# Kernel optimization log

Hardware: AMD Instinct MI355X
Metric: run time of the kernel (lower is better)

The kernel has to match this reference:

```python
import jax, jax.numpy as jnp
import numpy as np

EMBED = 384
N_HEADS = 6
HEAD_SIZE = EMBED // N_HEADS
B, T = 4, 2048
EPS = 1e-5


def _layernorm(x, g, b):
    mu = jnp.mean(x, axis=-1, keepdims=True)
    var = jnp.mean(jnp.square(x - mu), axis=-1, keepdims=True)
    return (x - mu) * jax.lax.rsqrt(var + EPS) * g + b


def setup_inputs() -> dict:
    key = jax.random.key(0)
    ks = jax.random.split(key, 6)
    s = 0.02
    return {
        "x": jax.random.normal(ks[0], (B, T, EMBED), jnp.float32),
        "Wq": jax.random.normal(ks[1], (N_HEADS, HEAD_SIZE, EMBED), jnp.float32) * s,
        "Wo": jax.random.normal(ks[2], (EMBED, EMBED), jnp.float32) * s,
        "bo": jnp.zeros((EMBED,), jnp.float32),
        "W1": jax.random.normal(ks[3], (EMBED, EMBED), jnp.float32) * s,
        "b1": jnp.zeros((EMBED,), jnp.float32),
        "W2": jax.random.normal(ks[4], (EMBED, EMBED), jnp.float32) * s,
        "b2": jnp.zeros((EMBED,), jnp.float32),
        "g1": jnp.ones((EMBED,), jnp.float32),
        "be1": jnp.zeros((EMBED,), jnp.float32),
        "g2": jnp.ones((EMBED,), jnp.float32),
        "be2": jnp.zeros((EMBED,), jnp.float32),
    }


def reference(x, Wq, Wo, bo, W1, b1, W2, b2, g1, be1, g2, be2):
    # NOTE: original Head uses self.query for q, k AND v (a bug we reproduce):
    # q = k = v = x @ Wq^T per head.
    q = jnp.einsum("bte,hde->bhtd", x, Wq)  # [B,H,T,D]
    scale = HEAD_SIZE ** -0.5
    scores = jnp.einsum("bhtd,bhsd->bhts", q, q) * scale  # [B,H,T,T]
    # torch.tril zeros the upper triangle, then masked_fill(tmp==0, -inf)
    tril = jnp.tril(jnp.ones((T, T), bool))
    scores = jnp.where(tril, scores, 0.0)
    scores = jnp.where(scores == 0.0, -jnp.inf, scores)
    attn = jax.nn.softmax(scores, axis=-1)
    head_out = jnp.einsum("bhts,bhsd->bhtd", attn, q)  # [B,H,T,D]
    cat = head_out.transpose(0, 2, 1, 3).reshape(B, T, EMBED)  # concat heads
    sa = cat @ Wo.T + bo
    x = _layernorm(x + sa, g1, be1)
    ff = jax.nn.relu(x @ W1.T + b1) @ W2.T + b2
    return _layernorm(x + ff, g2, be2)
```

## Files before the change

kernel.cpp:

```cpp
#include <hip/hip_runtime.h>
#include <math.h>

#define BB 4
#define TT 2048
#define EE 384
#define HH 6
#define DD 64
#define MM (BB*TT)

typedef __attribute__((ext_vector_type(8))) short bf16x8;
typedef __attribute__((ext_vector_type(4))) float f32x4;

__device__ __forceinline__ unsigned short f2bf(float f) {
    unsigned int u = __float_as_uint(f);
    u = (u + 0x7FFFu + ((u >> 16) & 1u)) >> 16;
    return (unsigned short)u;
}
__device__ __forceinline__ float bf2f(unsigned short u) {
    return __uint_as_float(((unsigned int)u) << 16);
}
__device__ __forceinline__ unsigned int pk2(float a, float b) {
    return (unsigned int)f2bf(a) | ((unsigned int)f2bf(b) << 16);
}
__device__ __forceinline__ unsigned int cvtpk(float lo, float hi) {
    unsigned int r;
    asm("v_cvt_pk_bf16_f32 %0, %1, %2" : "=v"(r) : "v"(lo), "v"(hi));
    return r;
}

__global__ __launch_bounds__(256) void k_cvt(const float* __restrict__ wq,
                                             const float* __restrict__ wo,
                                             const float* __restrict__ w1,
                                             const float* __restrict__ w2,
                                             unsigned short* __restrict__ wqb,
                                             unsigned short* __restrict__ wob,
                                             unsigned short* __restrict__ w1b,
                                             unsigned short* __restrict__ w2b)
{
    int wi = blockIdx.x / 144, off = (blockIdx.x % 144) * 256;
    const float* s4[4] = {wq, wo, w1, w2};
    unsigned short* d4[4] = {wqb, wob, w1b, w2b};
    const float* src = s4[wi]; unsigned short* dst = d4[wi];
    int i = off + threadIdx.x;
    float4 v = ((const float4*)src)[i];
    uint2 o; o.x = pk2(v.x, v.y); o.y = pk2(v.z, v.w);
    ((uint2*)dst)[i] = o;
}

__global__ __launch_bounds__(256, 2) void k_qgemm(const float* __restrict__ x,
                                                  const unsigned short* __restrict__ W,
                                                  unsigned short* __restrict__ qbf,
                                                  unsigned short* __restrict__ qbfT)
{
    __shared__ unsigned short Xs[32][396];
    __shared__ unsigned short Ts[32][200];
    const int tid = threadIdx.x;
    const int w = tid >> 6, lane = tid & 63;
    const int fr = lane & 15, quad = lane >> 4;
    const int m0 = blockIdx.x * 32;
    const int n0 = blockIdx.y * 192 + w * 48;
    const unsigned short* Wp = W + (size_t)(n0 + fr) * EE + quad * 8;

    {
        const float* xp = x + (size_t)m0 * EE;
        #pragma unroll
        for (int it = 0; it < 12; it++) {
            int idx = it * 1024 + tid * 4;
            int row = idx / EE, col = idx % EE;
            float4 v = *(const float4*)(xp + idx);
            uint2 o; o.x = pk2(v.x, v.y); o.y = pk2(v.z, v.w);
            *(uint2*)&Xs[row][col] = o;
        }
    }

    f32x4 acc[2][3];
    bf16x8 bc[3], bn[3];
    #pragma unroll
    for (int mt = 0; mt < 2; mt++)
        #pragma unroll
        for (int nt = 0; nt < 3; nt++) acc[mt][nt] = (f32x4){0.f, 0.f, 0.f, 0.f};
    #pragma unroll
    for (int nt = 0; nt < 3; nt++) bc[nt] = *(const bf16x8*)(Wp + (size_t)nt * 16 * EE);
    __syncthreads();

    #pragma unroll
    for (int k0 = 0; k0 < 12; k0++) {
        if (k0 < 11) {
            #pragma unroll
            for (int nt = 0; nt < 3; nt++)
                bn[nt] = *(const bf16x8*)(Wp + (size_t)nt * 16 * EE + (k0 + 1) * 32);
        }
        bf16x8 a0 = *(const bf16x8*)&Xs[fr][k0 * 32 + quad * 8];
        bf16x8 a1 = *(const bf16x8*)&Xs[16 + fr][k0 * 32 + quad * 8];
        #pragma unroll
        for (int nt = 0; nt < 3; nt++) {
            acc[0][nt] = __builtin_amdgcn_mfma_f32_16x16x32_bf16(a0, bc[nt], acc[0][nt], 0, 0, 0);
            acc[1][nt] = __builtin_amdgcn_mfma_f32_16x16x32_bf16(a1, bc[nt], acc[1][nt], 0, 0, 0);
        }
        #pragma unroll
        for (int nt = 0; nt < 3; nt++) bc[nt] = bn[nt];
    }

    const int bglob = m0 >> 11, t0 = m0 & 2047;
    #pragma unroll
    for (int nt = 0; nt < 3; nt++) {
        int nl = w * 48 + nt * 16 + fr;
        int n = blockIdx.y * 192 + nl;
        int h = n >> 6, d = n & 63;
        #pragma unroll
        for (int mt = 0; mt < 2; mt++)
            #pragma unroll
            for (int r = 0; r < 4; r++) {
                int ml = mt * 16 + quad * 4 + r;
                unsigned short bf = f2bf(acc[mt][nt][r]);
                qbf[((size_t)(bglob * HH + h) * TT + t0 + ml) * DD + d] = bf;
                Ts[ml][nl] = bf;
            }
    }
    __syncthreads();
    if (tid < 192) {
        int nl = tid;
        int n = blockIdx.y * 192 + nl;
        int h = n >> 6, d = n & 63;
        unsigned short tmp[32];
        #pragma unroll
        for (int i = 0; i < 32; i++) tmp[i] = Ts[i][nl];
        unsigned short* dst = qbfT + ((size_t)(bglob * HH + h) * DD + d) * TT + t0;
        *(uint4*)(dst)      = *(const uint4*)&tmp[0];
        *(uint4*)(dst + 8)  = *(const uint4*)&tmp[8];
        *(uint4*)(dst + 16) = *(const uint4*)&tmp[16];
        *(uint4*)(dst + 24) = *(const uint4*)&tmp[24];
    }
}

__global__ __launch_bounds__(256, 4) void k_attn(const unsigned short* __restrict__ qbf,
                                                 const unsigned short* __restrict__ qbfT,
                                                 unsigned short* __restrict__ cat)
{
    __shared__ unsigned short Ks[2][64][72];
    __shared__ unsigned short Vs[2][64][72];
    __shared__ unsigned short Ps[32][72];
    __shared__ float lsc[32];
    float (*Oc)[68] = (float(*)[68])&Ks[0][0][0];

    const int id = blockIdx.x;
    const int xcd = id & 7, j = id >> 3;
    const int bh = xcd * 3 + (j % 3);
    const int p = j / 3;
    const int bb = bh / HH, hh = bh % HH;
    const int tid = threadIdx.x;
    const int w = tid >> 6, lane = tid & 63;
    const int qhalf = w & 1, keyhalf = w >> 1;
    const int fr = lane & 15, quad = lane >> 4;
    const int fc = quad * 8;
    const unsigned short* qb  = qbf  + (size_t)bh * TT * DD;
    const unsigned short* qtb = qbfT + (size_t)bh * DD * TT;
    const int lr = tid >> 2, lc = (tid & 3) * 16;
    const float EXSC = 0.18033688011112042f;

    #pragma unroll 1
    for (int ph = 0; ph < 2; ph++) {
        const int tile = ph ? (63 - p) : p;
        const int m0 = tile * 32;
        const int nkt = (tile >> 1) + 1;

        uint4 kr0, kr1, vr0, vr1;
        {
            const unsigned short* kp = qb + (size_t)lr * DD + lc;
            kr0 = *(const uint4*)(kp);
            kr1 = *(const uint4*)(kp + 8);
            const unsigned short* vp = qtb + (size_t)lr * TT + lc;
            vr0 = *(const uint4*)(vp);
            vr1 = *(const uint4*)(vp + 8);
        }
        const unsigned short* qp = qb + (size_t)(m0 + qhalf * 16 + fr) * DD + fc;
        const bf16x8 qA0 = *(const bf16x8*)(qp);
        const bf16x8 qA1 = *(const bf16x8*)(qp + 32);

        __syncthreads();
        *(uint4*)&Ks[0][lr][lc]     = kr0;
        *(uint4*)&Ks[0][lr][lc + 8] = kr1;
        *(uint4*)&Vs[0][lr][lc]     = vr0;
        *(uint4*)&Vs[0][lr][lc + 8] = vr1;
        __syncthreads();

        f32x4 accO[4];
        #pragma unroll
        for (int dt = 0; dt < 4; dt++) accO[dt] = (f32x4){0.f, 0.f, 0.f, 0.f};
        float ls[4] = {0.f, 0.f, 0.f, 0.f};
        const int rowbase = m0 + qhalf * 16 + quad * 4;
        const int prow = qhalf * 16 + quad * 4;

        for (int kt = 0; kt < nkt; kt++) {
            const int cur = kt & 1;
            const int s0 = kt * 64;
            if (kt < nkt - 1) {
                const unsigned short* kp = qb + (size_t)(s0 + 64 + lr) * DD + lc;
                kr0 = *(const uint4*)(kp);
                kr1 = *(const uint4*)(kp + 8);
                const unsigned short* vp = qtb + (size_t)lr * TT + s0 + 64 + lc;
                vr0 = *(const uint4*)(vp);
                vr1 = *(const uint4*)(vp + 8);
            }

            f32x4 S[2];
            #pragma unroll
            for (int nt = 0; nt < 2; nt++) {
                f32x4 acc = (f32x4){0.f, 0.f, 0.f, 0.f};
                bf16x8 b0 = *(const bf16x8*)&Ks[cur][keyhalf * 32 + nt * 16 + fr][fc];
                acc = __builtin_amdgcn_mfma_f32_16x16x32_bf16(qA0, b0, acc, 0, 0, 0);
                bf16x8 b1 = *(const bf16x8*)&Ks[cur][keyhalf * 32 + nt * 16 + fr][fc + 32];
                acc = __builtin_amdgcn_mfma_f32_16x16x32_bf16(qA1, b1, acc, 0, 0, 0);
                S[nt] = acc;
            }

            const bool edge = (kt == nkt - 1);
            #pragma unroll
            for (int nt = 0; nt < 2; nt++) {
                const int col = keyhalf * 32 + nt * 16 + fr;
                float pv[4];
                if (edge) {
                    const int jg = s0 + col;
                    #pragma unroll
                    for (int r = 0; r < 4; r++) {
                        float s = S[nt][r];
                        pv[r] = (jg <= rowbase + r && s != 0.0f)
                                ? __builtin_amdgcn_exp2f(s * EXSC) : 0.0f;
                        ls[r] += pv[r];
                    }
                } else {
                    #pragma unroll
                    for (int r = 0; r < 4; r++) {
                        float s = S[nt][r];
                        pv[r] = (s != 0.0f) ? __builtin_amdgcn_exp2f(s * EXSC) : 0.0f;
                        ls[r] += pv[r];
                    }
                }
                unsigned int pk0 = cvtpk(pv[0], pv[1]);
                unsigned int pk1 = cvtpk(pv[2], pv[3]);
                Ps[prow + 0][col] = (unsigned short)(pk0);
                Ps[prow + 1][col] = (unsigned short)(pk0 >> 16);
                Ps[prow + 2][col] = (unsigned short)(pk1);
                Ps[prow + 3][col] = (unsigned short)(pk1 >> 16);
            }

            bf16x8 pA = *(const bf16x8*)&Ps[qhalf * 16 + fr][keyhalf * 32 + fc];
            #pragma unroll
            for (int dt = 0; dt < 4; dt++) {
                bf16x8 v0 = *(const bf16x8*)&Vs[cur][dt * 16 + fr][keyhalf * 32 + fc];
                accO[dt] = __builtin_amdgcn_mfma_f32_16x16x32_bf16(pA, v0, accO[dt], 0, 0, 0);
            }

            if (kt < nkt - 1) {
                *(uint4*)&Ks[cur ^ 1][lr][lc]     = kr0;
                *(uint4*)&Ks[cur ^ 1][lr][lc + 8] = kr1;
                *(uint4*)&Vs[cur ^ 1][lr][lc]     = vr0;
                *(uint4*)&Vs[cur ^ 1][lr][lc + 8] = vr1;
                __syncthreads();
            }
        }

        __syncthreads();
        #pragma unroll
        for (int r = 0; r < 4; r++) {
            #pragma unroll
            for (int o = 1; o < 16; o <<= 1) ls[r] += __shfl_xor(ls[r], o, 64);
        }
        if (keyhalf == 1) {
            #pragma unroll
            for (int dt = 0; dt < 4; dt++)
                #pragma unroll
                for (int r = 0; r < 4; r++)
                    Oc[prow + r][dt * 16 + fr] = accO[dt][r];
            if (fr == 0) {
                #pragma unroll
                for (int r = 0; r < 4; r++) lsc[prow + r] = ls[r];
            }
        }
        __syncthreads();
        if (keyhalf == 0) {
            float il[4];
            #pragma unroll
            for (int r = 0; r < 4; r++) il[r] = 1.0f / (ls[r] + lsc[prow + r]);
            #pragma unroll
            for (int dt = 0; dt < 4; dt++) {
                #pragma unroll
                for (int r = 0; r < 4; r++) {
                    float o = accO[dt][r] + Oc[prow + r][dt * 16 + fr];
                    int t = rowbase + r;
                    cat[((size_t)bb * TT + t) * EE + hh * DD + dt * 16 + fr] =
                        f2bf(o * il[r]);
                }
            }
        }
    }
}

__global__ __launch_bounds__(512, 2) void k_ffn(const unsigned short* __restrict__ catb,
                                                const unsigned short* __restrict__ wob,
                                                const float* __restrict__ bo,
                                                const float* __restrict__ x,
                                                const float* __restrict__ g1,
                                                const float* __restrict__ be1,
                                                const unsigned short* __restrict__ w1b,
                                                const float* __restrict__ b1,
                                                const unsigned short* __restrict__ w2b,
                                                const float* __restrict__ b2,
                                                const float* __restrict__ g2,
                                                const float* __restrict__ be2,
                                                float* __restrict__ out)
{
    __shared__ unsigned short X1s[32][392];
    __shared__ unsigned short H1s[32][392];
    __shared__ float ssum[32][8];
    __shared__ float ssq[32][8];
    const int tid = threadIdx.x;
    const int w = tid >> 6, lane = tid & 63;
    const int fr = lane & 15, quad = lane >> 4;
    const int m0 = blockIdx.x * 32;
    const int n0 = w * 48;

    f32x4 acc[2][3];
    bf16x8 bc[3], bn[3];
    const unsigned short* Wp1 = w1b + (size_t)(n0 + fr) * EE + quad * 8;
    const unsigned short* Wp2 = w2b + (size_t)(n0 + fr) * EE + quad * 8;

    {
        const unsigned short* Ap0 = catb + (size_t)(m0 + fr) * EE + quad * 8;
        const unsigned short* Ap1 = Ap0 + 16 * EE;
        const unsigned short* Wp = wob + (size_t)(n0 + fr) * EE + quad * 8;
        #pragma unroll
        for (int mt = 0; mt < 2; mt++)
            #pragma unroll
            for (int nt = 0; nt < 3; nt++) acc[mt][nt] = (f32x4){0.f, 0.f, 0.f, 0.f};
        #pragma unroll
        for (int nt = 0; nt < 3; nt++) bc[nt] = *(const bf16x8*)(Wp + (size_t)nt * 16 * EE);
        #pragma unroll
        for (int k0 = 0; k0 < 12; k0++) {
            if (k0 < 11) {
                #pragma unroll
                for (int nt = 0; nt < 3; nt++)
                    bn[nt] = *(const bf16x8*)(Wp + (size_t)nt * 16 * EE + (k0 + 1) * 32);
            }
            bf16x8 a0 = *(const bf16x8*)(Ap0 + k0 * 32);
            bf16x8 a1 = *(const bf16x8*)(Ap1 + k0 * 32);
            #pragma unroll
            for (int nt = 0; nt < 3; nt++) {
                acc[0][nt] = __builtin_amdgcn_mfma_f32_16x16x32_bf16(a0, bc[nt], acc[0][nt], 0, 0, 0);
                acc[1][nt] = __builtin_amdgcn_mfma_f32_16x16x32_bf16(a1, bc[nt], acc[1][nt], 0, 0, 0);
            }
            #pragma unroll
            for (int nt = 0; nt < 3; nt++) bc[nt] = bn[nt];
        }
    }
    #pragma unroll
    for (int nt = 0; nt < 3; nt++) bc[nt] = *(const bf16x8*)(Wp1 + (size_t)nt * 16 * EE);
    {
        float s1[2][4] = {{0.f,0.f,0.f,0.f},{0.f,0.f,0.f,0.f}};
        float s2[2][4] = {{0.f,0.f,0.f,0.f},{0.f,0.f,0.f,0.f}};
        #pragma unroll
        for (int nt = 0; nt < 3; nt++) {
            int n = n0 + nt * 16 + fr;
            float bv = bo[n];
            #pragma unroll
            for (int mt = 0; mt < 2; mt++)
                #pragma unroll
                for (int r = 0; r < 4; r++) {
                    float v = acc[mt][nt][r] + bv
                            + x[(size_t)(m0 + mt * 16 + quad * 4 + r) * EE + n];
                    acc[mt][nt][r] = v;
                    s1[mt][r] += v;
                    s2[mt][r] += v * v;
                }
        }
        #pragma unroll
        for (int mt = 0; mt < 2; mt++)
            #pragma unroll
            for (int r = 0; r < 4; r++) {
                #pragma unroll
                for (int o = 1; o < 16; o <<= 1) {
                    s1[mt][r] += __shfl_xor(s1[mt][r], o, 64);
                    s2[mt][r] += __shfl_xor(s2[mt][r], o, 64);
                }
            }
        if (fr == 0) {
            #pragma unroll
            for (int mt = 0; mt < 2; mt++)
                #pragma unroll
                for (int r = 0; r < 4; r++) {
                    ssum[mt * 16 + quad * 4 + r][w] = s1[mt][r];
                    ssq [mt * 16 + quad * 4 + r][w] = s2[mt][r];
                }
        }
    }
    __syncthreads();
    {
        #pragma unroll
        for (int mt = 0; mt < 2; mt++) {
            float mu[4], rs[4];
            #pragma unroll
            for (int r = 0; r < 4; r++) {
                int row = mt * 16 + quad * 4 + r;
                float t1 = 0.f, t2 = 0.f;
                #pragma unroll
                for (int q = 0; q < 8; q++) { t1 += ssum[row][q]; t2 += ssq[row][q]; }
                mu[r] = t1 * (1.0f / EE);
                float var = t2 * (1.0f / EE) - mu[r] * mu[r];
                rs[r] = rsqrtf(var + 1e-5f);
            }
            #pragma unroll
            for (int nt = 0; nt < 3; nt++) {
                int n = n0 + nt * 16 + fr;
                float gv = g1[n], bev = be1[n];
                #pragma unroll
                for (int r = 0; r < 4; r++) {
                    float v = (acc[mt][nt][r] - mu[r]) * rs[r] * gv + bev;
                    X1s[mt * 16 + quad * 4 + r][n] = f2bf(v);
                }
            }
        }
    }
    __syncthreads();

    {
        #pragma unroll
        for (int mt = 0; mt < 2; mt++)
            #pragma unroll
            for (int nt = 0; nt < 3; nt++) acc[mt][nt] = (f32x4){0.f, 0.f, 0.f, 0.f};
        #pragma unroll
        for (int k0 = 0; k0 < 12; k0++) {
            if (k0 < 11) {
                #pragma unroll
                for (int nt = 0; nt < 3; nt++)
                    bn[nt] = *(const bf16x8*)(Wp1 + (size_t)nt * 16 * EE + (k0 + 1) * 32);
            }
            bf16x8 a0 = *(const bf16x8*)&X1s[fr][k0 * 32 + quad * 8];
            bf16x8 a1 = *(const bf16x8*)&X1s[16 + fr][k0 * 32 + quad * 8];
            #pragma unroll
            for (int nt = 0; nt < 3; nt++) {
                acc[0][nt] = __builtin_amdgcn_mfma_f32_16x16x32_bf16(a0, bc[nt], acc[0][nt], 0, 0, 0);
                acc[1][nt] = __builtin_amdgcn_mfma_f32_16x16x32_bf16(a1, bc[nt], acc[1][nt], 0, 0, 0);
            }
            #pragma unroll
            for (int nt = 0; nt < 3; nt++) bc[nt] = bn[nt];
        }
        #pragma unroll
        for (int nt = 0; nt < 3; nt++) bc[nt] = *(const bf16x8*)(Wp2 + (size_t)nt * 16 * EE);
        #pragma unroll
        for (int nt = 0; nt < 3; nt++) {
            int n = n0 + nt * 16 + fr;
            float bv = b1[n];
            #pragma unroll
            for (int mt = 0; mt < 2; mt++)
                #pragma unroll
                for (int r = 0; r < 4; r++)
                    H1s[mt * 16 + quad * 4 + r][n] = f2bf(fmaxf(acc[mt][nt][r] + bv, 0.0f));
        }
    }
    __syncthreads();

    {
        #pragma unroll
        for (int mt = 0; mt < 2; mt++)
            #pragma unroll
            for (int nt = 0; nt < 3; nt++) acc[mt][nt] = (f32x4){0.f, 0.f, 0.f, 0.f};
        #pragma unroll
        for (int k0 = 0; k0 < 12; k0++) {
            if (k0 < 11) {
                #pragma unroll
                for (int nt = 0; nt < 3; nt++)
                    bn[nt] = *(const bf16x8*)(Wp2 + (size_t)nt * 16 * EE + (k0 + 1) * 32);
            }
            bf16x8 a0 = *(const bf16x8*)&H1s[fr][k0 * 32 + quad * 8];
            bf16x8 a1 = *(const bf16x8*)&H1s[16 + fr][k0 * 32 + quad * 8];
            #pragma unroll
            for (int nt = 0; nt < 3; nt++) {
                acc[0][nt] = __builtin_amdgcn_mfma_f32_16x16x32_bf16(a0, bc[nt], acc[0][nt], 0, 0, 0);
                acc[1][nt] = __builtin_amdgcn_mfma_f32_16x16x32_bf16(a1, bc[nt], acc[1][nt], 0, 0, 0);
            }
            #pragma unroll
            for (int nt = 0; nt < 3; nt++) bc[nt] = bn[nt];
        }
    }
    {
        float s1[2][4] = {{0.f,0.f,0.f,0.f},{0.f,0.f,0.f,0.f}};
        float s2[2][4] = {{0.f,0.f,0.f,0.f},{0.f,0.f,0.f,0.f}};
        #pragma unroll
        for (int nt = 0; nt < 3; nt++) {
            int n = n0 + nt * 16 + fr;
            float bv = b2[n];
            #pragma unroll
            for (int mt = 0; mt < 2; mt++)
                #pragma unroll
                for (int r = 0; r < 4; r++) {
                    float v = acc[mt][nt][r] + bv + bf2f(X1s[mt * 16 + quad * 4 + r][n]);
                    acc[mt][nt][r] = v;
                    s1[mt][r] += v;
                    s2[mt][r] += v * v;
                }
        }
        #pragma unroll
        for (int mt = 0; mt < 2; mt++)
            #pragma unroll
            for (int r = 0; r < 4; r++) {
                #pragma unroll
                for (int o = 1; o < 16; o <<= 1) {
                    s1[mt][r] += __shfl_xor(s1[mt][r], o, 64);
                    s2[mt][r] += __shfl_xor(s2[mt][r], o, 64);
                }
            }
        if (fr == 0) {
            #pragma unroll
            for (int mt = 0; mt < 2; mt++)
                #pragma unroll
                for (int r = 0; r < 4; r++) {
                    ssum[mt * 16 + quad * 4 + r][w] = s1[mt][r];
                    ssq [mt * 16 + quad * 4 + r][w] = s2[mt][r];
                }
        }
    }
    __syncthreads();
    {
        #pragma unroll
        for (int mt = 0; mt < 2; mt++) {
            float mu[4], rs[4];
            #pragma unroll
            for (int r = 0; r < 4; r++) {
                int row = mt * 16 + quad * 4 + r;
                float u1 = 0.f, u2 = 0.f;
                #pragma unroll
                for (int q = 0; q < 8; q++) { u1 += ssum[row][q]; u2 += ssq[row][q]; }
                mu[r] = u1 * (1.0f / EE);
                float var = u2 * (1.0f / EE) - mu[r] * mu[r];
                rs[r] = rsqrtf(var + 1e-5f);
            }
            #pragma unroll
            for (int nt = 0; nt < 3; nt++) {
                int n = n0 + nt * 16 + fr;
                float gv = g2[n], bev = be2[n];
                #pragma unroll
                for (int r = 0; r < 4; r++)
                    out[(size_t)(m0 + mt * 16 + quad * 4 + r) * EE + n] =
                        (acc[mt][nt][r] - mu[r]) * rs[r] * gv + bev;
            }
        }
    }
}

extern "C" void kernel_launch(void* const* d_in, const int* in_sizes, int n_in,
                              void* d_out, int out_size, void* d_ws, size_t ws_size,
                              hipStream_t stream) {
    (void)in_sizes; (void)n_in; (void)out_size; (void)ws_size;
    const float* x   = (const float*)d_in[0];
    const float* Wq  = (const float*)d_in[1];
    const float* Wo  = (const float*)d_in[2];
    const float* bo  = (const float*)d_in[3];
    const float* W1  = (const float*)d_in[4];
    const float* b1  = (const float*)d_in[5];
    const float* W2  = (const float*)d_in[6];
    const float* b2  = (const float*)d_in[7];
    const float* g1  = (const float*)d_in[8];
    const float* be1 = (const float*)d_in[9];
    const float* g2  = (const float*)d_in[10];
    const float* be2 = (const float*)d_in[11];
    float* out = (float*)d_out;

    float* ws = (float*)d_ws;
    const size_t SZ = (size_t)MM * EE;
    float* S1 = ws + SZ;
    float* S2 = ws + 2 * SZ;
    float* S3 = ws + 3 * SZ;

    unsigned short* qbf  = (unsigned short*)S1;
    unsigned short* qbfT = qbf + (size_t)BB * HH * TT * DD;
    unsigned short* catb = (unsigned short*)S2;
    unsigned short* wqb  = (unsigned short*)S3;
    unsigned short* wob  = wqb + (size_t)EE * EE;
    unsigned short* w1b  = wob + (size_t)EE * EE;
    unsigned short* w2b  = w1b + (size_t)EE * EE;

    k_cvt<<<dim3(4 * 144), dim3(256), 0, stream>>>(Wq, Wo, W1, W2, wqb, wob, w1b, w2b);
    k_qgemm<<<dim3(MM / 32, 2), dim3(256), 0, stream>>>(x, wqb, qbf, qbfT);
    k_attn<<<dim3(768), dim3(256), 0, stream>>>(qbf, qbfT, catb);
    k_ffn<<<dim3(MM / 32), dim3(512), 0, stream>>>(catb, wob, bo, x, g1, be1,
                                                   w1b, b1, w2b, b2, g2, be2, out);
}
```

Baseline: 174.5 us.

## Load attention K/V MFMA fragments directly from global, dropping LDS staging

The attention kernel no longer stages K and V tiles through double-buffered shared memory. Each wave loads its own MFMA B-operand fragments straight from global memory into registers and prefetches the next key tile's fragments, so the per-iteration block barrier disappears. The P scratch tile and the output-combine buffer get their own padded shared arrays. In exchange, waves that share keys fetch them redundantly through the cache, global-load latency is less hidden, and register pressure rises.

```diff
diff --git a/kernel.cpp b/kernel.cpp
--- a/kernel.cpp
+++ b/kernel.cpp
@@ -137,11 +137,9 @@
                                                  const unsigned short* __restrict__ qbfT,
                                                  unsigned short* __restrict__ cat)
 {
-    __shared__ unsigned short Ks[2][64][72];
-    __shared__ unsigned short Vs[2][64][72];
-    __shared__ unsigned short Ps[32][72];
+    __shared__ unsigned short Ps[32][76];
+    __shared__ float Oc[32][69];
     __shared__ float lsc[32];
-    float (*Oc)[68] = (float(*)[68])&Ks[0][0][0];
 
     const int id = blockIdx.x;
     const int xcd = id & 7, j = id >> 3;
@@ -155,8 +153,10 @@
     const int fc = quad * 8;
     const unsigned short* qb  = qbf  + (size_t)bh * TT * DD;
     const unsigned short* qtb = qbfT + (size_t)bh * DD * TT;
-    const int lr = tid >> 2, lc = (tid & 3) * 16;
     const float EXSC = 0.18033688011112042f;
+
+    const unsigned short* kfb = qb  + (size_t)(keyhalf * 32 + fr) * DD + fc;
+    const unsigned short* vfb = qtb + (size_t)fr * TT + keyhalf * 32 + fc;
 
     #pragma unroll 1
     for (int ph = 0; ph < 2; ph++) {
@@ -164,25 +164,20 @@
         const int m0 = tile * 32;
         const int nkt = (tile >> 1) + 1;
 
-        uint4 kr0, kr1, vr0, vr1;
-        {
-            const unsigned short* kp = qb + (size_t)lr * DD + lc;
-            kr0 = *(const uint4*)(kp);
-            kr1 = *(const uint4*)(kp + 8);
-            const unsigned short* vp = qtb + (size_t)lr * TT + lc;
-            vr0 = *(const uint4*)(vp);
-            vr1 = *(const uint4*)(vp + 8);
-        }
+        __syncthreads();
+
         const unsigned short* qp = qb + (size_t)(m0 + qhalf * 16 + fr) * DD + fc;
         const bf16x8 qA0 = *(const bf16x8*)(qp);
         const bf16x8 qA1 = *(const bf16x8*)(qp + 32);
 
-        __syncthreads();
-        *(uint4*)&Ks[0][lr][lc]     = kr0;
-        *(uint4*)&Ks[0][lr][lc + 8] = kr1;
-        *(uint4*)&Vs[0][lr][lc]     = vr0;
-        *(uint4*)&Vs[0][lr][lc + 8] = vr1;
-        __syncthreads();
+        bf16x8 kc0 = *(const bf16x8*)(kfb);
+        bf16x8 kc1 = *(const bf16x8*)(kfb + 32);
+        bf16x8 kc2 = *(const bf16x8*)(kfb + 16 * DD);
+        bf16x8 kc3 = *(const bf16x8*)(kfb + 16 * DD + 32);
+        bf16x8 vc0 = *(const bf16x8*)(vfb);
+        bf16x8 vc1 = *(const bf16x8*)(vfb + 16 * TT);
+        bf16x8 vc2 = *(const bf16x8*)(vfb + 32 * TT);
+        bf16x8 vc3 = *(const bf16x8*)(vfb + 48 * TT);
 
         f32x4 accO[4];
         #pragma unroll
@@ -190,77 +185,84 @@
         float ls[4] = {0.f, 0.f, 0.f, 0.f};
         const int rowbase = m0 + qhalf * 16 + quad * 4;
         const int prow = qhalf * 16 + quad * 4;
+        const int col0 = keyhalf * 32 + fr;
 
         for (int kt = 0; kt < nkt; kt++) {
-            const int cur = kt & 1;
             const int s0 = kt * 64;
-            if (kt < nkt - 1) {
-                const unsigned short* kp = qb + (size_t)(s0 + 64 + lr) * DD + lc;
-                kr0 = *(const uint4*)(kp);
-                kr1 = *(const uint4*)(kp + 8);
-                const unsigned short* vp = qtb + (size_t)lr * TT + s0 + 64 + lc;
-                vr0 = *(const uint4*)(vp);
-                vr1 = *(const uint4*)(vp + 8);
-            }
-
-            f32x4 S[2];
-            #pragma unroll
-            for (int nt = 0; nt < 2; nt++) {
-                f32x4 acc = (f32x4){0.f, 0.f, 0.f, 0.f};
-                bf16x8 b0 = *(const bf16x8*)&Ks[cur][keyhalf * 32 + nt * 16 + fr][fc];
-                acc = __builtin_amdgcn_mfma_f32_16x16x32_bf16(qA0, b0, acc, 0, 0, 0);
-                bf16x8 b1 = *(const bf16x8*)&Ks[cur][keyhalf * 32 + nt * 16 + fr][fc + 32];
-                acc = __builtin_amdgcn_mfma_f32_16x16x32_bf16(qA1, b1, acc, 0, 0, 0);
-                S[nt] = acc;
-            }
-
-            const bool edge = (kt == nkt - 1);
-            #pragma unroll
-            for (int nt = 0; nt < 2; nt++) {
-                const int col = keyhalf * 32 + nt * 16 + fr;
-                float pv[4];
-                if (edge) {
-                    const int jg = s0 + col;
-                    #pragma unroll
-                    for (int r = 0; r < 4; r++) {
-                        float s = S[nt][r];
-                        pv[r] = (jg <= rowbase + r && s != 0.0f)
-                                ? __builtin_amdgcn_exp2f(s * EXSC) : 0.0f;
-                        ls[r] += pv[r];
-                    }
-                } else {
-                    #pragma unroll
-                    for (int r = 0; r < 4; r++) {
-                        float s = S[nt][r];
-                        pv[r] = (s != 0.0f) ? __builtin_amdgcn_exp2f(s * EXSC) : 0.0f;
-                        ls[r] += pv[r];
-                    }
-                }
-                unsigned int pk0 = cvtpk(pv[0], pv[1]);
-                unsigned int pk1 = cvtpk(pv[2], pv[3]);
-                Ps[prow + 0][col] = (unsigned short)(pk0);
-                Ps[prow + 1][col] = (unsigned short)(pk0 >> 16);
-                Ps[prow + 2][col] = (unsigned short)(pk1);
-                Ps[prow + 3][col] = (unsigned short)(pk1 >> 16);
+
+            f32x4 S0 = (f32x4){0.f, 0.f, 0.f, 0.f};
+            f32x4 S1 = (f32x4){0.f, 0.f, 0.f, 0.f};
+            S0 = __builtin_amdgcn_mfma_f32_16x16x32_bf16(qA0, kc0, S0, 0, 0, 0);
+            S0 = __builtin_amdgcn_mfma_f32_16x16x32_bf16(qA1, kc1, S0, 0, 0, 0);
+            S1 = __builtin_amdgcn_mfma_f32_16x16x32_bf16(qA0, kc2, S1, 0, 0, 0);
+            S1 = __builtin_amdgcn_mfma_f32_16x16x32_bf16(qA1, kc3, S1, 0, 0, 0);
+
+            bf16x8 kn0, kn1, kn2, kn3;
+            const bool more = (kt < nkt - 1);
+            if (more) {
+                const unsigned short* kp = kfb + (size_t)(s0 + 64) * DD;
+                kn0 = *(const bf16x8*)(kp);
+                kn1 = *(const bf16x8*)(kp + 32);
+                kn2 = *(const bf16x8*)(kp + 16 * DD);
+                kn3 = *(const bf16x8*)(kp + 16 * DD + 32);
+            }
+
+            float pv0[4], pv1[4];
+            if (kt == nkt - 1) {
+                const int jg0 = s0 + col0;
+                #pragma unroll
+                for (int r = 0; r < 4; r++) {
+                    float s = S0[r];
+                    pv0[r] = (jg0 <= rowbase + r && s != 0.0f)
+                             ? __builtin_amdgcn_exp2f(s * EXSC) : 0.0f;
+                    ls[r] += pv0[r];
+                    s = S1[r];
+                    pv1[r] = (jg0 + 16 <= rowbase + r && s != 0.0f)
+                             ? __builtin_amdgcn_exp2f(s * EXSC) : 0.0f;
+                    ls[r] += pv1[r];
+                }
+            } else {
+                #pragma unroll
+                for (int r = 0; r < 4; r++) {
+                    float s = S0[r];
+                    pv0[r] = (s != 0.0f) ? __builtin_amdgcn_exp2f(s * EXSC) : 0.0f;
+                    ls[r] += pv0[r];
+                    s = S1[r];
+                    pv1[r] = (s != 0.0f) ? __builtin_amdgcn_exp2f(s * EXSC) : 0.0f;
+                    ls[r] += pv1[r];
+                }
+            }
+            {
+                unsigned int a0 = cvtpk(pv0[0], pv0[1]);
+                unsigned int a1 = cvtpk(pv0[2], pv0[3]);
+                unsigned int b0 = cvtpk(pv1[0], pv1[1]);
+                unsigned int b1 = cvtpk(pv1[2], pv1[3]);
+                Ps[prow + 0][col0]      = (unsigned short)(a0);
+                Ps[prow + 1][col0]      = (unsigned short)(a0 >> 16);
+                Ps[prow + 2][col0]      = (unsigned short)(a1);
+                Ps[prow + 3][col0]      = (unsigned short)(a1 >> 16);
+                Ps[prow + 0][col0 + 16] = (unsigned short)(b0);
+                Ps[prow + 1][col0 + 16] = (unsigned short)(b0 >> 16);
+                Ps[prow + 2][col0 + 16] = (unsigned short)(b1);
+                Ps[prow + 3][col0 + 16] = (unsigned short)(b1 >> 16);
             }
 
             bf16x8 pA = *(const bf16x8*)&Ps[qhalf * 16 + fr][keyhalf * 32 + fc];
-            #pragma unroll
-            for (int dt = 0; dt < 4; dt++) {
-                bf16x8 v0 = *(const bf16x8*)&Vs[cur][dt * 16 + fr][keyhalf * 32 + fc];
-                accO[dt] = __builtin_amdgcn_mfma_f32_16x16x32_bf16(pA, v0, accO[dt], 0, 0, 0);
-            }
-
-            if (kt < nkt - 1) {
-                *(uint4*)&Ks[cur ^ 1][lr][lc]     = kr0;
-                *(uint4*)&Ks[cur ^ 1][lr][lc + 8] = kr1;
-                *(uint4*)&Vs[cur ^ 1][lr][lc]     = vr0;
-                *(uint4*)&Vs[cur ^ 1][lr][lc + 8] = vr1;
-                __syncthreads();
-            }
-        }
-
-        __syncthreads();
+            accO[0] = __builtin_amdgcn_mfma_f32_16x16x32_bf16(pA, vc0, accO[0], 0, 0, 0);
+            accO[1] = __builtin_amdgcn_mfma_f32_16x16x32_bf16(pA, vc1, accO[1], 0, 0, 0);
+            accO[2] = __builtin_amdgcn_mfma_f32_16x16x32_bf16(pA, vc2, accO[2], 0, 0, 0);
+            accO[3] = __builtin_amdgcn_mfma_f32_16x16x32_bf16(pA, vc3, accO[3], 0, 0, 0);
+
+            if (more) {
+                const unsigned short* vp = vfb + s0 + 64;
+                vc0 = *(const bf16x8*)(vp);
+                vc1 = *(const bf16x8*)(vp + 16 * TT);
+                vc2 = *(const bf16x8*)(vp + 32 * TT);
+                vc3 = *(const bf16x8*)(vp + 48 * TT);
+                kc0 = kn0; kc1 = kn1; kc2 = kn2; kc3 = kn3;
+            }
+        }
+
         #pragma unroll
         for (int r = 0; r < 4; r++) {
             #pragma unroll
```

Result: slower. 227.7 us (+30.5%).
